# Kernel optimization log

Measured on AMD Instinct MI355X. Metric: run time of the kernel, lower is better.

Reference implementation:

```python
import jax, jax.numpy as jnp
import numpy as np


def _nearest(img, cy, cx):
    # PyTorch F.grid_sample(mode='nearest', align_corners=False, padding_mode='zeros').
    # img: [B,C,H,W]; cy,cx: [B,N] normalized coords in [-1,1] (cy->H axis, cx->W axis).
    B, C, H, W = img.shape
    iy = jnp.rint((cy + 1.0) * H / 2.0 - 0.5)  # unnormalize then nearbyint
    ix = jnp.rint((cx + 1.0) * W / 2.0 - 0.5)
    valid = (iy >= 0) & (iy < H) & (ix >= 0) & (ix < W)
    flat = (jnp.clip(iy, 0, H - 1).astype(jnp.int32) * W
            + jnp.clip(ix, 0, W - 1).astype(jnp.int32))  # [B,N]
    g = jnp.take_along_axis(img.reshape(B, C, H * W), flat[:, None, :], axis=2)  # [B,C,N]
    g = jnp.where(valid[:, None, :], g, 0.0)
    return g.transpose(0, 2, 1)  # [B,N,C]


def setup_inputs() -> dict:
    key = jax.random.key(0)
    ks = jax.random.split(key, 16)
    B, N = 2, 16384
    h, w = 64, 64       # LR feat / lr_guide resolution
    H, W = 256, 256     # HR guide resolution
    Cf, Cg = 128, 128   # feat_dim, guide_dim
    inp = {
        'feat': jax.random.normal(ks[0], (B, Cf, h, w), jnp.float32),
        'coord': jax.random.uniform(ks[1], (B, N, 2), jnp.float32) * 2.0 - 1.0,
        'hr_guide': jax.random.normal(ks[2], (B, Cg, H, W), jnp.float32),
        'lr_guide': jax.random.normal(ks[3], (B, Cg, h, w), jnp.float32),
    }
    dims = [386, 1024, 512, 256, 128, 2]  # imnet_in_dim -> hidden_list -> out_dim
    for i in range(5):
        fan_in, fan_out = dims[i], dims[i + 1]
        scale = np.sqrt(2.0 / fan_in).astype(np.float32)
        inp[f'W{i}'] = jax.random.normal(ks[4 + i], (fan_out, fan_in), jnp.float32) * scale
        inp[f'b{i}'] = jnp.zeros((fan_out,), jnp.float32)
    return inp


def reference(feat, coord, hr_guide, lr_guide, W0, b0, W1, b1, W2, b2, W3, b3, W4, b4):
    b, c, h, w = feat.shape
    # make_coord((h,w), flatten=False).permute(2,0,1): channel 0 = y (h axis), 1 = x (w axis)
    ys = -1.0 + 2.0 * (jnp.arange(h, dtype=jnp.float32) + 0.5) / h
    xs = -1.0 + 2.0 * (jnp.arange(w, dtype=jnp.float32) + 0.5) / w
    fc = jnp.stack([jnp.broadcast_to(ys[:, None], (h, w)),
                    jnp.broadcast_to(xs[None, :], (h, w))], 0)[None]  # [1,2,h,w]
    fc = jnp.broadcast_to(fc, (b, 2, h, w))

    # coord.flip(-1) as grid -> grid x = coord[...,1] (W axis), grid y = coord[...,0] (H axis)
    q_guide_hr = _nearest(hr_guide, coord[..., 0], coord[..., 1])  # [B,N,Cg]

    # 4 offsets (vx,vy) in [-1,1]x[-1,1], scaled by rx=1/h, ry=1/w (loop order of torch code)
    offs = jnp.array([[-1., -1.], [-1., 1.], [1., -1.], [1., 1.]], jnp.float32)
    offs = offs * jnp.array([1.0 / h, 1.0 / w], jnp.float32)
    cK = coord[None] + offs[:, None, None, :]  # [4,B,N,2]

    samp = jax.vmap(_nearest, in_axes=(None, 0, 0))
    q_feat = samp(feat, cK[..., 0], cK[..., 1])      # [4,B,N,Cf]
    q_coord = samp(fc, cK[..., 0], cK[..., 1])       # [4,B,N,2]
    q_lr = samp(lr_guide, cK[..., 0], cK[..., 1])    # [4,B,N,Cg]

    rel = (coord[None] - q_coord) * jnp.array([float(h), float(w)], jnp.float32)  # [4,B,N,2]
    qg_hr = jnp.broadcast_to(q_guide_hr[None], q_lr.shape)
    inp = jnp.concatenate([q_feat, qg_hr, qg_hr - q_lr, rel], axis=-1)  # [4,B,N,386]

    x = inp
    for Wl, bl in ((W0, b0), (W1, b1), (W2, b2), (W3, b3)):
        x = jax.nn.relu(x @ Wl.T + bl)
    preds = x @ W4.T + b4                      # [4,B,N,2]
    preds = jnp.moveaxis(preds, 0, -1)         # [B,N,2,4]
    wgt = jax.nn.softmax(preds[:, :, 1, :], axis=-1)
    return jnp.sum(preds[:, :, 0, :] * wgt, axis=-1, keepdims=True)  # [B,N,1]
```

## Files before the change

kernel.cpp:

```cpp
#include <hip/hip_runtime.h>
#include <cstdint>

typedef __attribute__((ext_vector_type(8))) _Float16 half8;
typedef __attribute__((ext_vector_type(16))) float   f32x16;

#define BN 2
#define NN 16384
#define FH 64
#define FW 64
#define GH 256
#define GW 256
#define CC 128
#define M_TOTAL (4*BN*NN)
#define MROWS 64
#define NBLK (M_TOTAL/MROWS)

#define SX  456
#define SHC 520
#define S2H 520
#define S3  264
#define S4  136
#define OFF_HC 29184
#define OFF_H3 62464
#define LDS_ELEMS 79360

#define MFMA(a,b,c) __builtin_amdgcn_mfma_f32_32x32x16_f16((a),(b),(c),0,0,0)

static __device__ __forceinline__ f32x16 zero16() {
  f32x16 z;
#pragma unroll
  for (int i = 0; i < 16; ++i) z[i] = 0.f;
  return z;
}
static __device__ __forceinline__ half8 zero8() {
  half8 z;
#pragma unroll
  for (int e = 0; e < 8; ++e) z[e] = (_Float16)0.f;
  return z;
}

template<int NB>
static __device__ __forceinline__ void ldA2(half8 (&A0)[NB], half8 (&A1)[NB],
    const _Float16* wa, const _Float16* wb, int t) {
#pragma unroll
  for (int i = 0; i < NB; ++i) {
    const int kt = t * NB + i;
    A0[i] = *(const half8*)(wa + kt * 512);
    A1[i] = *(const half8*)(wb + kt * 512);
  }
}
template<int NB>
static __device__ __forceinline__ void ldA1(half8 (&A)[NB], const _Float16* wa, int t) {
#pragma unroll
  for (int i = 0; i < NB; ++i) A[i] = *(const half8*)(wa + (t * NB + i) * 512);
}
template<int NB>
static __device__ __forceinline__ void ldB2(half8 (&B0)[NB], half8 (&B1)[NB],
    const _Float16* p0, const _Float16* p1, int t) {
#pragma unroll
  for (int i = 0; i < NB; ++i) {
    const int kt = t * NB + i;
    B0[i] = *(const half8*)(p0 + kt * 16);
    B1[i] = *(const half8*)(p1 + kt * 16);
  }
}
template<int NB>
static __device__ __forceinline__ void ldB1(half8 (&B)[NB], const _Float16* p, int t) {
#pragma unroll
  for (int i = 0; i < NB; ++i) B[i] = *(const half8*)(p + (t * NB + i) * 16);
}

template<int NB>
static __device__ __forceinline__ void mm_22(f32x16& a00, f32x16& a01, f32x16& a10, f32x16& a11,
    const half8 (&A0)[NB], const half8 (&A1)[NB], const half8 (&B0)[NB], const half8 (&B1)[NB]) {
  __builtin_amdgcn_sched_barrier(0);
  __builtin_amdgcn_s_setprio(1);
#pragma unroll
  for (int i = 0; i < NB; ++i) {
    a00 = MFMA(A0[i], B0[i], a00);
    a01 = MFMA(A0[i], B1[i], a01);
    a10 = MFMA(A1[i], B0[i], a10);
    a11 = MFMA(A1[i], B1[i], a11);
  }
  __builtin_amdgcn_s_setprio(0);
  __builtin_amdgcn_sched_barrier(0);
}
template<int NB>
static __device__ __forceinline__ void mm_12(f32x16& lo, f32x16& hi,
    const half8 (&A)[NB], const half8 (&B0)[NB], const half8 (&B1)[NB]) {
  __builtin_amdgcn_sched_barrier(0);
  __builtin_amdgcn_s_setprio(1);
#pragma unroll
  for (int i = 0; i < NB; ++i) {
    lo = MFMA(A[i], B0[i], lo);
    hi = MFMA(A[i], B1[i], hi);
  }
  __builtin_amdgcn_s_setprio(0);
  __builtin_amdgcn_sched_barrier(0);
}
template<int NB>
static __device__ __forceinline__ void mm_11(f32x16& acc,
    const half8 (&A)[NB], const half8 (&B)[NB]) {
  __builtin_amdgcn_sched_barrier(0);
  __builtin_amdgcn_s_setprio(1);
#pragma unroll
  for (int i = 0; i < NB; ++i) acc = MFMA(A[i], B[i], acc);
  __builtin_amdgcn_s_setprio(0);
  __builtin_amdgcn_sched_barrier(0);
}

__global__ void pack_w(const float* __restrict__ wsrc, _Float16* __restrict__ out,
                       int NT, int K, int KT) {
  int idx = blockIdx.x * 256 + threadIdx.x;
  int total = NT * KT * 64;
  if (idx >= total) return;
  int l = idx & 63;
  int t = idx >> 6;
  int kt = t % KT;
  int jt = t / KT;
  int row = jt * 32 + (l & 31);
  int k0 = kt * 16 + (l >> 5) * 8;
  _Float16* o = out + (size_t)idx * 8;
#pragma unroll
  for (int e = 0; e < 8; ++e) {
    int k = k0 + e;
    float v = (k < K) ? wsrc[(size_t)row * K + k] : 0.f;
    o[e] = (_Float16)v;
  }
}

__global__ void transpose_to_hwc(const float* __restrict__ in, _Float16* __restrict__ out,
                                 int C, int HH, int WW) {
  __shared__ float tile[32][33];
  const int xt = blockIdx.x, ct = blockIdx.y;
  const int bb = blockIdx.z / HH, y = blockIdx.z % HH;
  const int tx = threadIdx.x, ty = threadIdx.y;
  const int x0 = xt * 32, c0 = ct * 32;
#pragma unroll
  for (int i = 0; i < 4; ++i) {
    int c = c0 + ty + i * 8;
    tile[ty + i * 8][tx] = in[((size_t)(bb * C + c) * HH + y) * WW + x0 + tx];
  }
  __syncthreads();
#pragma unroll
  for (int i = 0; i < 4; ++i) {
    int x = x0 + ty + i * 8;
    out[((size_t)(bb * HH + y) * WW + x) * C + c0 + tx] = (_Float16)tile[tx][ty + i * 8];
  }
}

template<bool RELU>
static __device__ __forceinline__ void store_tile(const f32x16 acc, _Float16* lout, int ldo,
                                                  int row0, int col0,
                                                  const float* __restrict__ biasBase, int lane) {
  const int m = row0 + (lane & 31);
  const int s4 = (lane >> 5) * 4;
  _Float16* rp = lout + (size_t)m * ldo + col0 + s4;
  const float* bp = biasBase + s4;
#pragma unroll
  for (int g = 0; g < 4; ++g) {
    float4 bv = *(const float4*)(bp + 8 * g);
    union { _Float16 h[4]; unsigned long long u; } pk;
#pragma unroll
    for (int e = 0; e < 4; ++e) {
      float v = acc[4 * g + e] + ((const float*)&bv)[e];
      if (RELU) v = fmaxf(v, 0.f);
      pk.h[e] = (_Float16)v;
    }
    *(unsigned long long*)(rp + 8 * g) = pk.u;
  }
}

__global__ __launch_bounds__(512, 2) void jiif_main(
    const float* __restrict__ coord,
    const _Float16* __restrict__ featT, const _Float16* __restrict__ hrT,
    const _Float16* __restrict__ lrT,
    const _Float16* __restrict__ W0p, const _Float16* __restrict__ W1p,
    const _Float16* __restrict__ W2p, const _Float16* __restrict__ W3p,
    const float* __restrict__ b0, const float* __restrict__ b1,
    const float* __restrict__ b2, const float* __restrict__ b3,
    const float* __restrict__ W4, const float* __restrict__ b4,
    float* __restrict__ preds) {
  extern __shared__ _Float16 lds[];
  const int tid = threadIdx.x;
  const int w = tid >> 6, lane = tid & 63;
  const int m0 = blockIdx.x * MROWS;
  _Float16* X   = lds;
  _Float16* Hc  = lds + OFF_HC;
  _Float16* H2r = lds;
  _Float16* H3r = lds + OFF_H3;
  _Float16* H4r = lds;

  {
    const int r = tid >> 3;
    const int g = tid & 7;
    const int row = m0 + r;
    const int n = row & (NN - 1);
    const int bb = (row >> 14) & (BN - 1);
    const int k = row >> 15;
    const float c0 = coord[((size_t)bb * NN + n) * 2 + 0];
    const float c1 = coord[((size_t)bb * NN + n) * 2 + 1];
    const float cy = c0 + ((k < 2) ? -1.f : 1.f) * (1.f / FH);
    const float cx = c1 + ((k & 1) ? 1.f : -1.f) * (1.f / FW);
    const float fy = rintf((cy + 1.f) * (FH * 0.5f) - 0.5f);
    const float fx = rintf((cx + 1.f) * (FW * 0.5f) - 0.5f);
    const bool vF = (fy >= 0.f) && (fy < (float)FH) && (fx >= 0.f) && (fx < (float)FW);
    const int iy = max(0, min(FH - 1, (int)fy));
    const int ix = max(0, min(FW - 1, (int)fx));
    const float gy = rintf((c0 + 1.f) * (GH * 0.5f) - 0.5f);
    const float gx = rintf((c1 + 1.f) * (GW * 0.5f) - 0.5f);
    const bool vH = (gy >= 0.f) && (gy < (float)GH) && (gx >= 0.f) && (gx < (float)GW);
    const int jy = max(0, min(GH - 1, (int)gy));
    const int jx = max(0, min(GW - 1, (int)gx));
    const _Float16* fp = featT + (size_t)((bb * FH + iy) * FW + ix) * CC;
    const _Float16* lp = lrT  + (size_t)((bb * FH + iy) * FW + ix) * CC;
    const _Float16* hp = hrT  + (size_t)((bb * GH + jy) * GW + jx) * CC;
    _Float16* xr = X + (size_t)r * SX;
#pragma unroll
    for (int t = 0; t < 2; ++t) {
      const int c8 = g * 16 + t * 8;
      half8 fv = vF ? *(const half8*)(fp + c8) : zero8();
      half8 lv = vF ? *(const half8*)(lp + c8) : zero8();
      half8 hv = vH ? *(const half8*)(hp + c8) : zero8();
      *(half8*)(xr + c8) = fv;
      *(half8*)(xr + CC + c8) = hv;
      half8 dv = hv - lv;
      *(half8*)(xr + 2 * CC + c8) = dv;
    }
    *(unsigned long long*)(xr + 384 + g * 8) = 0ull;
    *(unsigned long long*)(xr + 384 + g * 8 + 4) = 0ull;
    if (g == 0) {
      const float qc0 = vF ? (-1.f + (float)(2 * iy + 1) * (1.f / FH)) : 0.f;
      const float qc1 = vF ? (-1.f + (float)(2 * ix + 1) * (1.f / FW)) : 0.f;
      xr[384] = (_Float16)((c0 - qc0) * (float)FH);
      xr[385] = (_Float16)((c1 - qc1) * (float)FW);
    }
  }
  __syncthreads();

  const int m31 = lane & 31;
  const int s8 = (lane >> 5) * 8;
  const _Float16* xb0 = X + (size_t)m31 * SX + s8;
  const _Float16* xb1 = xb0 + 32 * SX;
  const _Float16* hb0 = Hc + (size_t)m31 * SHC + s8;
  const _Float16* hb1 = hb0 + 32 * SHC;

  {
    f32x16 a00 = zero16(), a01 = zero16(), a10 = zero16(), a11 = zero16();
    const _Float16* wa = W0p + ((size_t)(2 * w) * 28 * 64 + lane) * 8;
    const _Float16* wb = wa + 28 * 512;
    half8 pA0[2], pA1[2], pB0[2], pB1[2], qA0[2], qA1[2], qB0[2], qB1[2];
    ldA2<2>(pA0, pA1, wa, wb, 0); ldB2<2>(pB0, pB1, xb0, xb1, 0);
    ldA2<2>(qA0, qA1, wa, wb, 1); ldB2<2>(qB0, qB1, xb0, xb1, 1);
#pragma unroll 1
    for (int u = 0; u < 6; ++u) {
      mm_22<2>(a00, a01, a10, a11, pA0, pA1, pB0, pB1);
      ldA2<2>(pA0, pA1, wa, wb, 2 * u + 2); ldB2<2>(pB0, pB1, xb0, xb1, 2 * u + 2);
      mm_22<2>(a00, a01, a10, a11, qA0, qA1, qB0, qB1);
      ldA2<2>(qA0, qA1, wa, wb, 2 * u + 3); ldB2<2>(qB0, qB1, xb0, xb1, 2 * u + 3);
    }
    mm_22<2>(a00, a01, a10, a11, pA0, pA1, pB0, pB1);
    mm_22<2>(a00, a01, a10, a11, qA0, qA1, qB0, qB1);
    store_tile<true>(a00, Hc, SHC, 0,  (2 * w) * 32,     b0 + (2 * w) * 32,     lane);
    store_tile<true>(a01, Hc, SHC, 32, (2 * w) * 32,     b0 + (2 * w) * 32,     lane);
    store_tile<true>(a10, Hc, SHC, 0,  (2 * w + 1) * 32, b0 + (2 * w + 1) * 32, lane);
    store_tile<true>(a11, Hc, SHC, 32, (2 * w + 1) * 32, b0 + (2 * w + 1) * 32, lane);
  }
  __syncthreads();

  f32x16 a2_00 = zero16(), a2_01 = zero16(), a2_10 = zero16(), a2_11 = zero16();
  const _Float16* w1a = W1p + ((size_t)(2 * w) * 64 * 64 + lane) * 8;
  const _Float16* w1b = w1a + 64 * 512;
  {
    half8 sA0[2], sA1[2], sB0[2], sB1[2], tA0[2], tA1[2], tB0[2], tB1[2];
    ldA2<2>(sA0, sA1, w1a, w1b, 0); ldB2<2>(sB0, sB1, hb0, hb1, 0);
    ldA2<2>(tA0, tA1, w1a, w1b, 1); ldB2<2>(tB0, tB1, hb0, hb1, 1);
#pragma unroll 1
    for (int u = 0; u < 7; ++u) {
      mm_22<2>(a2_00, a2_01, a2_10, a2_11, sA0, sA1, sB0, sB1);
      ldA2<2>(sA0, sA1, w1a, w1b, 2 * u + 2); ldB2<2>(sB0, sB1, hb0, hb1, 2 * u + 2);
      mm_22<2>(a2_00, a2_01, a2_10, a2_11, tA0, tA1, tB0, tB1);
      ldA2<2>(tA0, tA1, w1a, w1b, 2 * u + 3); ldB2<2>(tB0, tB1, hb0, hb1, 2 * u + 3);
    }
    mm_22<2>(a2_00, a2_01, a2_10, a2_11, sA0, sA1, sB0, sB1);
    mm_22<2>(a2_00, a2_01, a2_10, a2_11, tA0, tA1, tB0, tB1);
  }
  __syncthreads();

  {
    f32x16 a00 = zero16(), a01 = zero16(), a10 = zero16(), a11 = zero16();
    const _Float16* wa = W0p + ((size_t)(16 + 2 * w) * 28 * 64 + lane) * 8;
    const _Float16* wb = wa + 28 * 512;
    half8 pA0[2], pA1[2], pB0[2], pB1[2], qA0[2], qA1[2], qB0[2], qB1[2];
    ldA2<2>(pA0, pA1, wa, wb, 0); ldB2<2>(pB0, pB1, xb0, xb1, 0);
    ldA2<2>(qA0, qA1, wa, wb, 1); ldB2<2>(qB0, qB1, xb0, xb1, 1);
#pragma unroll 1
    for (int u = 0; u < 6; ++u) {
      mm_22<2>(a00, a01, a10, a11, pA0, pA1, pB0, pB1);
      ldA2<2>(pA0, pA1, wa, wb, 2 * u + 2); ldB2<2>(pB0, pB1, xb0, xb1, 2 * u + 2);
      mm_22<2>(a00, a01, a10, a11, qA0, qA1, qB0, qB1);
      ldA2<2>(qA0, qA1, wa, wb, 2 * u + 3); ldB2<2>(qB0, qB1, xb0, xb1, 2 * u + 3);
    }
    mm_22<2>(a00, a01, a10, a11, pA0, pA1, pB0, pB1);
    mm_22<2>(a00, a01, a10, a11, qA0, qA1, qB0, qB1);
    store_tile<true>(a00, Hc, SHC, 0,  (2 * w) * 32,     b0 + 512 + (2 * w) * 32,     lane);
    store_tile<true>(a01, Hc, SHC, 32, (2 * w) * 32,     b0 + 512 + (2 * w) * 32,     lane);
    store_tile<true>(a10, Hc, SHC, 0,  (2 * w + 1) * 32, b0 + 512 + (2 * w + 1) * 32, lane);
    store_tile<true>(a11, Hc, SHC, 32, (2 * w + 1) * 32, b0 + 512 + (2 * w + 1) * 32, lane);
  }
  __syncthreads();

  {
    const _Float16* wa = w1a + 32 * 512;
    const _Float16* wb = w1b + 32 * 512;
    half8 sA0[2], sA1[2], sB0[2], sB1[2], tA0[2], tA1[2], tB0[2], tB1[2];
    ldA2<2>(sA0, sA1, wa, wb, 0); ldB2<2>(sB0, sB1, hb0, hb1, 0);
    ldA2<2>(tA0, tA1, wa, wb, 1); ldB2<2>(tB0, tB1, hb0, hb1, 1);
#pragma unroll 1
    for (int u = 0; u < 7; ++u) {
      mm_22<2>(a2_00, a2_01, a2_10, a2_11, sA0, sA1, sB0, sB1);
      ldA2<2>(sA0, sA1, wa, wb, 2 * u + 2); ldB2<2>(sB0, sB1, hb0, hb1, 2 * u + 2);
      mm_22<2>(a2_00, a2_01, a2_10, a2_11, tA0, tA1, tB0, tB1);
      ldA2<2>(tA0, tA1, wa, wb, 2 * u + 3); ldB2<2>(tB0, tB1, hb0, hb1, 2 * u + 3);
    }
    mm_22<2>(a2_00, a2_01, a2_10, a2_11, sA0, sA1, sB0, sB1);
    mm_22<2>(a2_00, a2_01, a2_10, a2_11, tA0, tA1, tB0, tB1);
  }
  __syncthreads();

  store_tile<true>(a2_00, H2r, S2H, 0,  (2 * w) * 32,     b1 + (2 * w) * 32,     lane);
  store_tile<true>(a2_01, H2r, S2H, 32, (2 * w) * 32,     b1 + (2 * w) * 32,     lane);
  store_tile<true>(a2_10, H2r, S2H, 0,  (2 * w + 1) * 32, b1 + (2 * w + 1) * 32, lane);
  store_tile<true>(a2_11, H2r, S2H, 32, (2 * w + 1) * 32, b1 + (2 * w + 1) * 32, lane);
  __syncthreads();

  {
    const _Float16* wb2 = W2p + ((size_t)w * 32 * 64 + lane) * 8;
    const _Float16* h2b0 = H2r + (size_t)m31 * S2H + s8;
    const _Float16* h2b1 = h2b0 + 32 * S2H;
    f32x16 a3lo = zero16(), a3hi = zero16();
    half8 sA[2], sB0[2], sB1[2], tA[2], tB0[2], tB1[2];
    ldA1<2>(sA, wb2, 0); ldB2<2>(sB0, sB1, h2b0, h2b1, 0);
    ldA1<2>(tA, wb2, 1); ldB2<2>(tB0, tB1, h2b0, h2b1, 1);
#pragma unroll 1
    for (int u = 0; u < 7; ++u) {
      mm_12<2>(a3lo, a3hi, sA, sB0, sB1);
      ldA1<2>(sA, wb2, 2 * u + 2); ldB2<2>(sB0, sB1, h2b0, h2b1, 2 * u + 2);
      mm_12<2>(a3lo, a3hi, tA, tB0, tB1);
      ldA1<2>(tA, wb2, 2 * u + 3); ldB2<2>(tB0, tB1, h2b0, h2b1, 2 * u + 3);
    }
    mm_12<2>(a3lo, a3hi, sA, sB0, sB1);
    mm_12<2>(a3lo, a3hi, tA, tB0, tB1);
    store_tile<true>(a3lo, H3r, S3, 0,  w * 32, b2 + w * 32, lane);
    store_tile<true>(a3hi, H3r, S3, 32, w * 32, b2 + w * 32, lane);
  }
  __syncthreads();

  {
    const int j3 = w & 3, mts = w >> 2;
    const _Float16* wb3 = W3p + ((size_t)j3 * 16 * 64 + lane) * 8;
    const _Float16* h3b = H3r + (size_t)(mts * 32 + m31) * S3 + s8;
    f32x16 a4 = zero16();
    half8 sA[4], sB[4], tA[4], tB[4];
    ldA1<4>(sA, wb3, 0); ldB1<4>(sB, h3b, 0);
    ldA1<4>(tA, wb3, 1); ldB1<4>(tB, h3b, 1);
    mm_11<4>(a4, sA, sB);
    ldA1<4>(sA, wb3, 2); ldB1<4>(sB, h3b, 2);
    mm_11<4>(a4, tA, tB);
    ldA1<4>(tA, wb3, 3); ldB1<4>(tB, h3b, 3);
    mm_11<4>(a4, sA, sB);
    mm_11<4>(a4, tA, tB);
    store_tile<true>(a4, H4r, S4, mts * 32, j3 * 32, b3 + j3 * 32, lane);
  }
  __syncthreads();

  {
    const int m = tid >> 3;
    const int sub = tid & 7;
    const int j = sub & 1;
    const int q = sub >> 1;
    const _Float16* h4 = H4r + (size_t)m * S4 + q * 32;
    const float* w4 = W4 + j * CC + q * 32;
    float s = 0.f;
#pragma unroll
    for (int cc = 0; cc < 32; ++cc) s += (float)h4[cc] * w4[cc];
    s += __shfl_xor(s, 2);
    s += __shfl_xor(s, 4);
    if (q == 0) preds[(size_t)(m0 + m) * 2 + j] = s + b4[j];
  }
}

__global__ void jiif_combine(const float* __restrict__ preds, float* __restrict__ out) {
  const int i = blockIdx.x * 256 + threadIdx.x;
  if (i >= BN * NN) return;
  float p0[4], p1[4];
#pragma unroll
  for (int k = 0; k < 4; ++k) {
    p0[k] = preds[((size_t)k * BN * NN + i) * 2 + 0];
    p1[k] = preds[((size_t)k * BN * NN + i) * 2 + 1];
  }
  float mx = fmaxf(fmaxf(p1[0], p1[1]), fmaxf(p1[2], p1[3]));
  float se = 0.f, so = 0.f;
#pragma unroll
  for (int k = 0; k < 4; ++k) {
    float e = expf(p1[k] - mx);
    se += e;
    so += p0[k] * e;
  }
  out[i] = so / se;
}

extern "C" void kernel_launch(void* const* d_in, const int* in_sizes, int n_in,
                              void* d_out, int out_size, void* d_ws, size_t ws_size,
                              hipStream_t stream) {
  const float* feat  = (const float*)d_in[0];
  const float* coord = (const float*)d_in[1];
  const float* hr    = (const float*)d_in[2];
  const float* lr    = (const float*)d_in[3];
  const float* W0 = (const float*)d_in[4];  const float* b0 = (const float*)d_in[5];
  const float* W1 = (const float*)d_in[6];  const float* b1 = (const float*)d_in[7];
  const float* W2 = (const float*)d_in[8];  const float* b2 = (const float*)d_in[9];
  const float* W3 = (const float*)d_in[10]; const float* b3 = (const float*)d_in[11];
  const float* W4 = (const float*)d_in[12]; const float* b4 = (const float*)d_in[13];

  char* ws = (char*)d_ws;
  _Float16* W0p   = (_Float16*)(ws + 0);
  _Float16* W1p   = (_Float16*)(ws + 917504);
  _Float16* W2p   = (_Float16*)(ws + 1966080);
  _Float16* W3p   = (_Float16*)(ws + 2228224);
  _Float16* featT = (_Float16*)(ws + 2293760);
  _Float16* hrT   = (_Float16*)(ws + 4390912);
  _Float16* lrT   = (_Float16*)(ws + 37945344);
  float* preds    = (float*)(ws + 40042496);
  if (ws_size < 41091072) return;

  pack_w<<<224, 256, 0, stream>>>(W0, W0p, 32, 386, 28);
  pack_w<<<256, 256, 0, stream>>>(W1, W1p, 16, 1024, 64);
  pack_w<<<64,  256, 0, stream>>>(W2, W2p, 8, 512, 32);
  pack_w<<<16,  256, 0, stream>>>(W3, W3p, 4, 256, 16);

  transpose_to_hwc<<<dim3(2, 4, 128), dim3(32, 8), 0, stream>>>(feat, featT, CC, FH, FW);
  transpose_to_hwc<<<dim3(8, 4, 512), dim3(32, 8), 0, stream>>>(hr,   hrT,   CC, GH, GW);
  transpose_to_hwc<<<dim3(2, 4, 128), dim3(32, 8), 0, stream>>>(lr,   lrT,   CC, FH, FW);

  (void)hipFuncSetAttribute((const void*)jiif_main,
                            hipFuncAttributeMaxDynamicSharedMemorySize, LDS_ELEMS * 2);
  jiif_main<<<NBLK, 512, LDS_ELEMS * 2, stream>>>(
      coord, featT, hrT, lrT, W0p, W1p, W2p, W3p, b0, b1, b2, b3, W4, b4, preds);

  jiif_combine<<<(BN * NN + 255) / 256, 256, 0, stream>>>(preds, (float*)d_out);
}
```

Measured before the change: 357.1 us.

## Double block to 1024 threads, give each wave one output column tile

The fused MLP block grows from 8 to 16 waves. Each wave now computes a single 32-column tile per layer instead of two, with mm_12 replacing mm_22. Layer 2 is split across both M halves, and the gather and final dot product are remapped to 16 threads per row. The aim is more waves to hide latency per block. The cost is that each weight fragment is reused across fewer MFMAs, so global weight loads per FLOP double, and occupancy moves from 2 blocks per CU to 1.

Result: slower. 434.4 us (+21.6%).

```diff
diff --git a/kernel.cpp b/kernel.cpp
--- a/kernel.cpp
+++ b/kernel.cpp
@@ -40,16 +40,6 @@
 }
 
 template<int NB>
-static __device__ __forceinline__ void ldA2(half8 (&A0)[NB], half8 (&A1)[NB],
-    const _Float16* wa, const _Float16* wb, int t) {
-#pragma unroll
-  for (int i = 0; i < NB; ++i) {
-    const int kt = t * NB + i;
-    A0[i] = *(const half8*)(wa + kt * 512);
-    A1[i] = *(const half8*)(wb + kt * 512);
-  }
-}
-template<int NB>
 static __device__ __forceinline__ void ldA1(half8 (&A)[NB], const _Float16* wa, int t) {
 #pragma unroll
   for (int i = 0; i < NB; ++i) A[i] = *(const half8*)(wa + (t * NB + i) * 512);
@@ -70,21 +60,6 @@
   for (int i = 0; i < NB; ++i) B[i] = *(const half8*)(p + (t * NB + i) * 16);
 }
 
-template<int NB>
-static __device__ __forceinline__ void mm_22(f32x16& a00, f32x16& a01, f32x16& a10, f32x16& a11,
-    const half8 (&A0)[NB], const half8 (&A1)[NB], const half8 (&B0)[NB], const half8 (&B1)[NB]) {
-  __builtin_amdgcn_sched_barrier(0);
-  __builtin_amdgcn_s_setprio(1);
-#pragma unroll
-  for (int i = 0; i < NB; ++i) {
-    a00 = MFMA(A0[i], B0[i], a00);
-    a01 = MFMA(A0[i], B1[i], a01);
-    a10 = MFMA(A1[i], B0[i], a10);
-    a11 = MFMA(A1[i], B1[i], a11);
-  }
-  __builtin_amdgcn_s_setprio(0);
-  __builtin_amdgcn_sched_barrier(0);
-}
 template<int NB>
 static __device__ __forceinline__ void mm_12(f32x16& lo, f32x16& hi,
     const half8 (&A)[NB], const half8 (&B0)[NB], const half8 (&B1)[NB]) {
@@ -171,7 +146,7 @@
   }
 }
 
-__global__ __launch_bounds__(512, 2) void jiif_main(
+__global__ __launch_bounds__(1024, 1) void jiif_main(
     const float* __restrict__ coord,
     const _Float16* __restrict__ featT, const _Float16* __restrict__ hrT,
     const _Float16* __restrict__ lrT,
@@ -192,8 +167,8 @@
   _Float16* H4r = lds;
 
   {
-    const int r = tid >> 3;
-    const int g = tid & 7;
+    const int r = tid >> 4;
+    const int g = tid & 15;
     const int row = m0 + r;
     const int n = row & (NN - 1);
     const int bb = (row >> 14) & (BN - 1);
@@ -216,19 +191,18 @@
     const _Float16* lp = lrT  + (size_t)((bb * FH + iy) * FW + ix) * CC;
     const _Float16* hp = hrT  + (size_t)((bb * GH + jy) * GW + jx) * CC;
     _Float16* xr = X + (size_t)r * SX;
-#pragma unroll
-    for (int t = 0; t < 2; ++t) {
-      const int c8 = g * 16 + t * 8;
-      half8 fv = vF ? *(const half8*)(fp + c8) : zero8();
-      half8 lv = vF ? *(const half8*)(lp + c8) : zero8();
-      half8 hv = vH ? *(const half8*)(hp + c8) : zero8();
-      *(half8*)(xr + c8) = fv;
-      *(half8*)(xr + CC + c8) = hv;
-      half8 dv = hv - lv;
-      *(half8*)(xr + 2 * CC + c8) = dv;
-    }
-    *(unsigned long long*)(xr + 384 + g * 8) = 0ull;
-    *(unsigned long long*)(xr + 384 + g * 8 + 4) = 0ull;
+    const int c8 = g * 8;
+    half8 fv = vF ? *(const half8*)(fp + c8) : zero8();
+    half8 lv = vF ? *(const half8*)(lp + c8) : zero8();
+    half8 hv = vH ? *(const half8*)(hp + c8) : zero8();
+    *(half8*)(xr + c8) = fv;
+    *(half8*)(xr + CC + c8) = hv;
+    half8 dv = hv - lv;
+    *(half8*)(xr + 2 * CC + c8) = dv;
+    if (g < 8) {
+      *(unsigned long long*)(xr + 384 + g * 8) = 0ull;
+      *(unsigned long long*)(xr + 384 + g * 8 + 4) = 0ull;
+    }
     if (g == 0) {
       const float qc0 = vF ? (-1.f + (float)(2 * iy + 1) * (1.f / FH)) : 0.f;
       const float qc1 = vF ? (-1.f + (float)(2 * ix + 1) * (1.f / FW)) : 0.f;
@@ -245,121 +219,111 @@
   const _Float16* hb0 = Hc + (size_t)m31 * SHC + s8;
   const _Float16* hb1 = hb0 + 32 * SHC;
 
-  {
-    f32x16 a00 = zero16(), a01 = zero16(), a10 = zero16(), a11 = zero16();
-    const _Float16* wa = W0p + ((size_t)(2 * w) * 28 * 64 + lane) * 8;
-    const _Float16* wb = wa + 28 * 512;
-    half8 pA0[2], pA1[2], pB0[2], pB1[2], qA0[2], qA1[2], qB0[2], qB1[2];
-    ldA2<2>(pA0, pA1, wa, wb, 0); ldB2<2>(pB0, pB1, xb0, xb1, 0);
-    ldA2<2>(qA0, qA1, wa, wb, 1); ldB2<2>(qB0, qB1, xb0, xb1, 1);
+  f32x16 a2_0 = zero16(), a2_1 = zero16();
+  const _Float16* w1a = W1p + ((size_t)w * 64 * 64 + lane) * 8;
+
+  {
+    f32x16 a0 = zero16(), a1 = zero16();
+    const _Float16* wa = W0p + ((size_t)w * 28 * 64 + lane) * 8;
+    half8 sA[2], sB0[2], sB1[2], tA[2], tB0[2], tB1[2];
+    ldA1<2>(sA, wa, 0); ldB2<2>(sB0, sB1, xb0, xb1, 0);
+    ldA1<2>(tA, wa, 1); ldB2<2>(tB0, tB1, xb0, xb1, 1);
 #pragma unroll 1
     for (int u = 0; u < 6; ++u) {
-      mm_22<2>(a00, a01, a10, a11, pA0, pA1, pB0, pB1);
-      ldA2<2>(pA0, pA1, wa, wb, 2 * u + 2); ldB2<2>(pB0, pB1, xb0, xb1, 2 * u + 2);
-      mm_22<2>(a00, a01, a10, a11, qA0, qA1, qB0, qB1);
-      ldA2<2>(qA0, qA1, wa, wb, 2 * u + 3); ldB2<2>(qB0, qB1, xb0, xb1, 2 * u + 3);
-    }
-    mm_22<2>(a00, a01, a10, a11, pA0, pA1, pB0, pB1);
-    mm_22<2>(a00, a01, a10, a11, qA0, qA1, qB0, qB1);
-    store_tile<true>(a00, Hc, SHC, 0,  (2 * w) * 32,     b0 + (2 * w) * 32,     lane);
-    store_tile<true>(a01, Hc, SHC, 32, (2 * w) * 32,     b0 + (2 * w) * 32,     lane);
-    store_tile<true>(a10, Hc, SHC, 0,  (2 * w + 1) * 32, b0 + (2 * w + 1) * 32, lane);
-    store_tile<true>(a11, Hc, SHC, 32, (2 * w + 1) * 32, b0 + (2 * w + 1) * 32, lane);
-  }
-  __syncthreads();
-
-  f32x16 a2_00 = zero16(), a2_01 = zero16(), a2_10 = zero16(), a2_11 = zero16();
-  const _Float16* w1a = W1p + ((size_t)(2 * w) * 64 * 64 + lane) * 8;
-  const _Float16* w1b = w1a + 64 * 512;
-  {
-    half8 sA0[2], sA1[2], sB0[2], sB1[2], tA0[2], tA1[2], tB0[2], tB1[2];
-    ldA2<2>(sA0, sA1, w1a, w1b, 0); ldB2<2>(sB0, sB1, hb0, hb1, 0);
-    ldA2<2>(tA0, tA1, w1a, w1b, 1); ldB2<2>(tB0, tB1, hb0, hb1, 1);
+      mm_12<2>(a0, a1, sA, sB0, sB1);
+      ldA1<2>(sA, wa, 2 * u + 2); ldB2<2>(sB0, sB1, xb0, xb1, 2 * u + 2);
+      mm_12<2>(a0, a1, tA, tB0, tB1);
+      ldA1<2>(tA, wa, 2 * u + 3); ldB2<2>(tB0, tB1, xb0, xb1, 2 * u + 3);
+    }
+    mm_12<2>(a0, a1, sA, sB0, sB1);
+    mm_12<2>(a0, a1, tA, tB0, tB1);
+    store_tile<true>(a0, Hc, SHC, 0,  w * 32, b0 + w * 32, lane);
+    store_tile<true>(a1, Hc, SHC, 32, w * 32, b0 + w * 32, lane);
+  }
+  __syncthreads();
+
+  {
+    half8 sA[2], sB0[2], sB1[2], tA[2], tB0[2], tB1[2];
+    ldA1<2>(sA, w1a, 0); ldB2<2>(sB0, sB1, hb0, hb1, 0);
+    ldA1<2>(tA, w1a, 1); ldB2<2>(tB0, tB1, hb0, hb1, 1);
 #pragma unroll 1
     for (int u = 0; u < 7; ++u) {
-      mm_22<2>(a2_00, a2_01, a2_10, a2_11, sA0, sA1, sB0, sB1);
-      ldA2<2>(sA0, sA1, w1a, w1b, 2 * u + 2); ldB2<2>(sB0, sB1, hb0, hb1, 2 * u + 2);
-      mm_22<2>(a2_00, a2_01, a2_10, a2_11, tA0, tA1, tB0, tB1);
-      ldA2<2>(tA0, tA1, w1a, w1b, 2 * u + 3); ldB2<2>(tB0, tB1, hb0, hb1, 2 * u + 3);
-    }
-    mm_22<2>(a2_00, a2_01, a2_10, a2_11, sA0, sA1, sB0, sB1);
-    mm_22<2>(a2_00, a2_01, a2_10, a2_11, tA0, tA1, tB0, tB1);
-  }
-  __syncthreads();
-
-  {
-    f32x16 a00 = zero16(), a01 = zero16(), a10 = zero16(), a11 = zero16();
-    const _Float16* wa = W0p + ((size_t)(16 + 2 * w) * 28 * 64 + lane) * 8;
-    const _Float16* wb = wa + 28 * 512;
-    half8 pA0[2], pA1[2], pB0[2], pB1[2], qA0[2], qA1[2], qB0[2], qB1[2];
-    ldA2<2>(pA0, pA1, wa, wb, 0); ldB2<2>(pB0, pB1, xb0, xb1, 0);
-    ldA2<2>(qA0, qA1, wa, wb, 1); ldB2<2>(qB0, qB1, xb0, xb1, 1);
+      mm_12<2>(a2_0, a2_1, sA, sB0, sB1);
+      ldA1<2>(sA, w1a, 2 * u + 2); ldB2<2>(sB0, sB1, hb0, hb1, 2 * u + 2);
+      mm_12<2>(a2_0, a2_1, tA, tB0, tB1);
+      ldA1<2>(tA, w1a, 2 * u + 3); ldB2<2>(tB0, tB1, hb0, hb1, 2 * u + 3);
+    }
+    mm_12<2>(a2_0, a2_1, sA, sB0, sB1);
+    mm_12<2>(a2_0, a2_1, tA, tB0, tB1);
+  }
+  __syncthreads();
+
+  {
+    f32x16 a0 = zero16(), a1 = zero16();
+    const _Float16* wa = W0p + ((size_t)(16 + w) * 28 * 64 + lane) * 8;
+    half8 sA[2], sB0[2], sB1[2], tA[2], tB0[2], tB1[2];
+    ldA1<2>(sA, wa, 0); ldB2<2>(sB0, sB1, xb0, xb1, 0);
+    ldA1<2>(tA, wa, 1); ldB2<2>(tB0, tB1, xb0, xb1, 1);
 #pragma unroll 1
     for (int u = 0; u < 6; ++u) {
-      mm_22<2>(a00, a01, a10, a11, pA0, pA1, pB0, pB1);
-      ldA2<2>(pA0, pA1, wa, wb, 2 * u + 2); ldB2<2>(pB0, pB1, xb0, xb1, 2 * u + 2);
-      mm_22<2>(a00, a01, a10, a11, qA0, qA1, qB0, qB1);
-      ldA2<2>(qA0, qA1, wa, wb, 2 * u + 3); ldB2<2>(qB0, qB1, xb0, xb1, 2 * u + 3);
-    }
-    mm_22<2>(a00, a01, a10, a11, pA0, pA1, pB0, pB1);
-    mm_22<2>(a00, a01, a10, a11, qA0, qA1, qB0, qB1);
-    store_tile<true>(a00, Hc, SHC, 0,  (2 * w) * 32,     b0 + 512 + (2 * w) * 32,     lane);
-    store_tile<true>(a01, Hc, SHC, 32, (2 * w) * 32,     b0 + 512 + (2 * w) * 32,     lane);
-    store_tile<true>(a10, Hc, SHC, 0,  (2 * w + 1) * 32, b0 + 512 + (2 * w + 1) * 32, lane);
-    store_tile<true>(a11, Hc, SHC, 32, (2 * w + 1) * 32, b0 + 512 + (2 * w + 1) * 32, lane);
+      mm_12<2>(a0, a1, sA, sB0, sB1);
+      ldA1<2>(sA, wa, 2 * u + 2); ldB2<2>(sB0, sB1, xb0, xb1, 2 * u + 2);
+      mm_12<2>(a0, a1, tA, tB0, tB1);
+      ldA1<2>(tA, wa, 2 * u + 3); ldB2<2>(tB0, tB1, xb0, xb1, 2 * u + 3);
+    }
+    mm_12<2>(a0, a1, sA, sB0, sB1);
+    mm_12<2>(a0, a1, tA, tB0, tB1);
+    store_tile<true>(a0, Hc, SHC, 0,  w * 32, b0 + 512 + w * 32, lane);
+    store_tile<true>(a1, Hc, SHC, 32, w * 32, b0 + 512 + w * 32, lane);
   }
   __syncthreads();
 
   {
     const _Float16* wa = w1a + 32 * 512;
-    const _Float16* wb = w1b + 32 * 512;
-    half8 sA0[2], sA1[2], sB0[2], sB1[2], tA0[2], tA1[2], tB0[2], tB1[2];
-    ldA2<2>(sA0, sA1, wa, wb, 0); ldB2<2>(sB0, sB1, hb0, hb1, 0);
-    ldA2<2>(tA0, tA1, wa, wb, 1); ldB2<2>(tB0, tB1, hb0, hb1, 1);
+    half8 sA[2], sB0[2], sB1[2], tA[2], tB0[2], tB1[2];
+    ldA1<2>(sA, wa, 0); ldB2<2>(sB0, sB1, hb0, hb1, 0);
+    ldA1<2>(tA, wa, 1); ldB2<2>(tB0, tB1, hb0, hb1, 1);
 #pragma unroll 1
     for (int u = 0; u < 7; ++u) {
-      mm_22<2>(a2_00, a2_01, a2_10, a2_11, sA0, sA1, sB0, sB1);
-      ldA2<2>(sA0, sA1, wa, wb, 2 * u + 2); ldB2<2>(sB0, sB1, hb0, hb1, 2 * u + 2);
-      mm_22<2>(a2_00, a2_01, a2_10, a2_11, tA0, tA1, tB0, tB1);
-      ldA2<2>(tA0, tA1, wa, wb, 2 * u + 3); ldB2<2>(tB0, tB1, hb0, hb1, 2 * u + 3);
-    }
-    mm_22<2>(a2_00, a2_01, a2_10, a2_11, sA0, sA1, sB0, sB1);
-    mm_22<2>(a2_00, a2_01, a2_10, a2_11, tA0, tA1, tB0, tB1);
-  }
-  __syncthreads();
-
-  store_tile<true>(a2_00, H2r, S2H, 0,  (2 * w) * 32,     b1 + (2 * w) * 32,     lane);
-  store_tile<true>(a2_01, H2r, S2H, 32, (2 * w) * 32,     b1 + (2 * w) * 32,     lane);
-  store_tile<true>(a2_10, H2r, S2H, 0,  (2 * w + 1) * 32, b1 + (2 * w + 1) * 32, lane);
-  store_tile<true>(a2_11, H2r, S2H, 32, (2 * w + 1) * 32, b1 + (2 * w + 1) * 32, lane);
-  __syncthreads();
-
-  {
-    const _Float16* wb2 = W2p + ((size_t)w * 32 * 64 + lane) * 8;
-    const _Float16* h2b0 = H2r + (size_t)m31 * S2H + s8;
-    const _Float16* h2b1 = h2b0 + 32 * S2H;
-    f32x16 a3lo = zero16(), a3hi = zero16();
-    half8 sA[2], sB0[2], sB1[2], tA[2], tB0[2], tB1[2];
-    ldA1<2>(sA, wb2, 0); ldB2<2>(sB0, sB1, h2b0, h2b1, 0);
-    ldA1<2>(tA, wb2, 1); ldB2<2>(tB0, tB1, h2b0, h2b1, 1);
+      mm_12<2>(a2_0, a2_1, sA, sB0, sB1);
+      ldA1<2>(sA, wa, 2 * u + 2); ldB2<2>(sB0, sB1, hb0, hb1, 2 * u + 2);
+      mm_12<2>(a2_0, a2_1, tA, tB0, tB1);
+      ldA1<2>(tA, wa, 2 * u + 3); ldB2<2>(tB0, tB1, hb0, hb1, 2 * u + 3);
+    }
+    mm_12<2>(a2_0, a2_1, sA, sB0, sB1);
+    mm_12<2>(a2_0, a2_1, tA, tB0, tB1);
+  }
+  __syncthreads();
+
+  store_tile<true>(a2_0, H2r, S2H, 0,  w * 32, b1 + w * 32, lane);
+  store_tile<true>(a2_1, H2r, S2H, 32, w * 32, b1 + w * 32, lane);
+  __syncthreads();
+
+  {
+    const _Float16* wb2 = W2p + ((size_t)(w & 7) * 32 * 64 + lane) * 8;
+    const int mts2 = w >> 3;
+    const _Float16* h2b = H2r + (size_t)(mts2 * 32 + m31) * S2H + s8;
+    f32x16 a3 = zero16();
+    half8 sA[2], sB[2], tA[2], tB[2];
+    ldA1<2>(sA, wb2, 0); ldB1<2>(sB, h2b, 0);
+    ldA1<2>(tA, wb2, 1); ldB1<2>(tB, h2b, 1);
 #pragma unroll 1
     for (int u = 0; u < 7; ++u) {
-      mm_12<2>(a3lo, a3hi, sA, sB0, sB1);
-      ldA1<2>(sA, wb2, 2 * u + 2); ldB2<2>(sB0, sB1, h2b0, h2b1, 2 * u + 2);
-      mm_12<2>(a3lo, a3hi, tA, tB0, tB1);
-      ldA1<2>(tA, wb2, 2 * u + 3); ldB2<2>(tB0, tB1, h2b0, h2b1, 2 * u + 3);
-    }
-    mm_12<2>(a3lo, a3hi, sA, sB0, sB1);
-    mm_12<2>(a3lo, a3hi, tA, tB0, tB1);
-    store_tile<true>(a3lo, H3r, S3, 0,  w * 32, b2 + w * 32, lane);
-    store_tile<true>(a3hi, H3r, S3, 32, w * 32, b2 + w * 32, lane);
-  }
-  __syncthreads();
-
-  {
-    const int j3 = w & 3, mts = w >> 2;
+      mm_11<2>(a3, sA, sB);
+      ldA1<2>(sA, wb2, 2 * u + 2); ldB1<2>(sB, h2b, 2 * u + 2);
+      mm_11<2>(a3, tA, tB);
+      ldA1<2>(tA, wb2, 2 * u + 3); ldB1<2>(tB, h2b, 2 * u + 3);
+    }
+    mm_11<2>(a3, sA, sB);
+    mm_11<2>(a3, tA, tB);
+    store_tile<true>(a3, H3r, S3, mts2 * 32, (w & 7) * 32, b2 + (w & 7) * 32, lane);
+  }
+  __syncthreads();
+
+  if (w < 8) {
+    const int j3 = w & 3, mts3 = w >> 2;
     const _Float16* wb3 = W3p + ((size_t)j3 * 16 * 64 + lane) * 8;
-    const _Float16* h3b = H3r + (size_t)(mts * 32 + m31) * S3 + s8;
+    const _Float16* h3b = H3r + (size_t)(mts3 * 32 + m31) * S3 + s8;
     f32x16 a4 = zero16();
     half8 sA[4], sB[4], tA[4], tB[4];
     ldA1<4>(sA, wb3, 0); ldB1<4>(sB, h3b, 0);
@@ -370,22 +334,23 @@
     ldA1<4>(tA, wb3, 3); ldB1<4>(tB, h3b, 3);
     mm_11<4>(a4, sA, sB);
     mm_11<4>(a4, tA, tB);
-    store_tile<true>(a4, H4r, S4, mts * 32, j3 * 32, b3 + j3 * 32, lane);
-  }
-  __syncthreads();
-
-  {
-    const int m = tid >> 3;
-    const int sub = tid & 7;
+    store_tile<true>(a4, H4r, S4, mts3 * 32, j3 * 32, b3 + j3 * 32, lane);
+  }
+  __syncthreads();
+
+  {
+    const int m = tid >> 4;
+    const int sub = tid & 15;
     const int j = sub & 1;
     const int q = sub >> 1;
-    const _Float16* h4 = H4r + (size_t)m * S4 + q * 32;
-    const float* w4 = W4 + j * CC + q * 32;
+    const _Float16* h4 = H4r + (size_t)m * S4 + q * 16;
+    const float* w4 = W4 + j * CC + q * 16;
     float s = 0.f;
 #pragma unroll
-    for (int cc = 0; cc < 32; ++cc) s += (float)h4[cc] * w4[cc];
+    for (int cc = 0; cc < 16; ++cc) s += (float)h4[cc] * w4[cc];
     s += __shfl_xor(s, 2);
     s += __shfl_xor(s, 4);
+    s += __shfl_xor(s, 8);
     if (q == 0) preds[(size_t)(m0 + m) * 2 + j] = s + b4[j];
   }
 }
@@ -445,7 +410,7 @@
 
   (void)hipFuncSetAttribute((const void*)jiif_main,
                             hipFuncAttributeMaxDynamicSharedMemorySize, LDS_ELEMS * 2);
-  jiif_main<<<NBLK, 512, LDS_ELEMS * 2, stream>>>(
+  jiif_main<<<NBLK, 1024, LDS_ELEMS * 2, stream>>>(
       coord, featT, hrT, lrT, W0p, W1p, W2p, W3p, b0, b1, b2, b3, W4, b4, preds);
 
   jiif_combine<<<(BN * NN + 255) / 256, 256, 0, stream>>>(preds, (float*)d_out);
```

## Stage layer-0/1 weight tiles via global_load_lds double buffer instead of registers

Applied to the files above, without the earlier changes.

Weight A-fragments for the first two MLP layers now stream from global memory directly into a per-wave LDS staging double buffer using global_load_lds, then get read from LDS, rather than being loaded into registers two k-steps ahead. The two chunk passes are folded into one loop over c, and waits use explicit vmcnt counters. The aim is to cut VGPR pressure and overlap weight fetch with MFMA work. The cost is extra LDS traffic, an extra LDS read per step, and a shallower prefetch of one k-step at a time, which may expose global latency.

After: 388.5 us. 1.09x slower.

```diff
diff --git a/kernel.cpp b/kernel.cpp
--- a/kernel.cpp
+++ b/kernel.cpp
@@ -39,16 +39,13 @@
   return z;
 }
 
-template<int NB>
-static __device__ __forceinline__ void ldA2(half8 (&A0)[NB], half8 (&A1)[NB],
-    const _Float16* wa, const _Float16* wb, int t) {
-#pragma unroll
-  for (int i = 0; i < NB; ++i) {
-    const int kt = t * NB + i;
-    A0[i] = *(const half8*)(wa + kt * 512);
-    A1[i] = *(const half8*)(wb + kt * 512);
-  }
-}
+typedef __attribute__((address_space(1))) const void gas_void;
+typedef __attribute__((address_space(3))) void las_void;
+static __device__ __forceinline__ void glds16(const _Float16* g, const _Float16* l) {
+  __builtin_amdgcn_global_load_lds((gas_void*)(uintptr_t)g,
+                                   (las_void*)(uint32_t)(uintptr_t)l, 16, 0, 0);
+}
+
 template<int NB>
 static __device__ __forceinline__ void ldA1(half8 (&A)[NB], const _Float16* wa, int t) {
 #pragma unroll
@@ -70,21 +67,6 @@
   for (int i = 0; i < NB; ++i) B[i] = *(const half8*)(p + (t * NB + i) * 16);
 }
 
-template<int NB>
-static __device__ __forceinline__ void mm_22(f32x16& a00, f32x16& a01, f32x16& a10, f32x16& a11,
-    const half8 (&A0)[NB], const half8 (&A1)[NB], const half8 (&B0)[NB], const half8 (&B1)[NB]) {
-  __builtin_amdgcn_sched_barrier(0);
-  __builtin_amdgcn_s_setprio(1);
-#pragma unroll
-  for (int i = 0; i < NB; ++i) {
-    a00 = MFMA(A0[i], B0[i], a00);
-    a01 = MFMA(A0[i], B1[i], a01);
-    a10 = MFMA(A1[i], B0[i], a10);
-    a11 = MFMA(A1[i], B1[i], a11);
-  }
-  __builtin_amdgcn_s_setprio(0);
-  __builtin_amdgcn_sched_barrier(0);
-}
 template<int NB>
 static __device__ __forceinline__ void mm_12(f32x16& lo, f32x16& hi,
     const half8 (&A)[NB], const half8 (&B0)[NB], const half8 (&B1)[NB]) {
@@ -190,6 +172,7 @@
   _Float16* H2r = lds;
   _Float16* H3r = lds + OFF_H3;
   _Float16* H4r = lds;
+  _Float16* stg = lds + OFF_H3 + (size_t)w * 2048;
 
   {
     const int r = tid >> 3;
@@ -240,93 +223,123 @@
 
   const int m31 = lane & 31;
   const int s8 = (lane >> 5) * 8;
+  const int lane8 = lane * 8;
   const _Float16* xb0 = X + (size_t)m31 * SX + s8;
   const _Float16* xb1 = xb0 + 32 * SX;
   const _Float16* hb0 = Hc + (size_t)m31 * SHC + s8;
   const _Float16* hb1 = hb0 + 32 * SHC;
 
-  {
-    f32x16 a00 = zero16(), a01 = zero16(), a10 = zero16(), a11 = zero16();
-    const _Float16* wa = W0p + ((size_t)(2 * w) * 28 * 64 + lane) * 8;
-    const _Float16* wb = wa + 28 * 512;
-    half8 pA0[2], pA1[2], pB0[2], pB1[2], qA0[2], qA1[2], qB0[2], qB1[2];
-    ldA2<2>(pA0, pA1, wa, wb, 0); ldB2<2>(pB0, pB1, xb0, xb1, 0);
-    ldA2<2>(qA0, qA1, wa, wb, 1); ldB2<2>(qB0, qB1, xb0, xb1, 1);
-#pragma unroll 1
-    for (int u = 0; u < 6; ++u) {
-      mm_22<2>(a00, a01, a10, a11, pA0, pA1, pB0, pB1);
-      ldA2<2>(pA0, pA1, wa, wb, 2 * u + 2); ldB2<2>(pB0, pB1, xb0, xb1, 2 * u + 2);
-      mm_22<2>(a00, a01, a10, a11, qA0, qA1, qB0, qB1);
-      ldA2<2>(qA0, qA1, wa, wb, 2 * u + 3); ldB2<2>(qB0, qB1, xb0, xb1, 2 * u + 3);
-    }
-    mm_22<2>(a00, a01, a10, a11, pA0, pA1, pB0, pB1);
-    mm_22<2>(a00, a01, a10, a11, qA0, qA1, qB0, qB1);
-    store_tile<true>(a00, Hc, SHC, 0,  (2 * w) * 32,     b0 + (2 * w) * 32,     lane);
-    store_tile<true>(a01, Hc, SHC, 32, (2 * w) * 32,     b0 + (2 * w) * 32,     lane);
-    store_tile<true>(a10, Hc, SHC, 0,  (2 * w + 1) * 32, b0 + (2 * w + 1) * 32, lane);
-    store_tile<true>(a11, Hc, SHC, 32, (2 * w + 1) * 32, b0 + (2 * w + 1) * 32, lane);
-  }
-  __syncthreads();
-
   f32x16 a2_00 = zero16(), a2_01 = zero16(), a2_10 = zero16(), a2_11 = zero16();
   const _Float16* w1a = W1p + ((size_t)(2 * w) * 64 * 64 + lane) * 8;
   const _Float16* w1b = w1a + 64 * 512;
-  {
-    half8 sA0[2], sA1[2], sB0[2], sB1[2], tA0[2], tA1[2], tB0[2], tB1[2];
-    ldA2<2>(sA0, sA1, w1a, w1b, 0); ldB2<2>(sB0, sB1, hb0, hb1, 0);
-    ldA2<2>(tA0, tA1, w1a, w1b, 1); ldB2<2>(tB0, tB1, hb0, hb1, 1);
+
 #pragma unroll 1
-    for (int u = 0; u < 7; ++u) {
-      mm_22<2>(a2_00, a2_01, a2_10, a2_11, sA0, sA1, sB0, sB1);
-      ldA2<2>(sA0, sA1, w1a, w1b, 2 * u + 2); ldB2<2>(sB0, sB1, hb0, hb1, 2 * u + 2);
-      mm_22<2>(a2_00, a2_01, a2_10, a2_11, tA0, tA1, tB0, tB1);
-      ldA2<2>(tA0, tA1, w1a, w1b, 2 * u + 3); ldB2<2>(tB0, tB1, hb0, hb1, 2 * u + 3);
-    }
-    mm_22<2>(a2_00, a2_01, a2_10, a2_11, sA0, sA1, sB0, sB1);
-    mm_22<2>(a2_00, a2_01, a2_10, a2_11, tA0, tA1, tB0, tB1);
-  }
-  __syncthreads();
-
-  {
+  for (int c = 0; c < 2; ++c) {
     f32x16 a00 = zero16(), a01 = zero16(), a10 = zero16(), a11 = zero16();
-    const _Float16* wa = W0p + ((size_t)(16 + 2 * w) * 28 * 64 + lane) * 8;
+    const _Float16* wa = W0p + ((size_t)(c * 16 + 2 * w) * 28 * 64 + lane) * 8;
     const _Float16* wb = wa + 28 * 512;
-    half8 pA0[2], pA1[2], pB0[2], pB1[2], qA0[2], qA1[2], qB0[2], qB1[2];
-    ldA2<2>(pA0, pA1, wa, wb, 0); ldB2<2>(pB0, pB1, xb0, xb1, 0);
-    ldA2<2>(qA0, qA1, wa, wb, 1); ldB2<2>(qB0, qB1, xb0, xb1, 1);
+    glds16(wa, stg);            glds16(wb, stg + 512);
+    glds16(wa + 512, stg + 1024); glds16(wb + 512, stg + 1536);
+    half8 B0c = *(const half8*)(xb0);
+    half8 B1c = *(const half8*)(xb1);
 #pragma unroll 1
-    for (int u = 0; u < 6; ++u) {
-      mm_22<2>(a00, a01, a10, a11, pA0, pA1, pB0, pB1);
-      ldA2<2>(pA0, pA1, wa, wb, 2 * u + 2); ldB2<2>(pB0, pB1, xb0, xb1, 2 * u + 2);
-      mm_22<2>(a00, a01, a10, a11, qA0, qA1, qB0, qB1);
-      ldA2<2>(qA0, qA1, wa, wb, 2 * u + 3); ldB2<2>(qB0, qB1, xb0, xb1, 2 * u + 3);
-    }
-    mm_22<2>(a00, a01, a10, a11, pA0, pA1, pB0, pB1);
-    mm_22<2>(a00, a01, a10, a11, qA0, qA1, qB0, qB1);
-    store_tile<true>(a00, Hc, SHC, 0,  (2 * w) * 32,     b0 + 512 + (2 * w) * 32,     lane);
-    store_tile<true>(a01, Hc, SHC, 32, (2 * w) * 32,     b0 + 512 + (2 * w) * 32,     lane);
-    store_tile<true>(a10, Hc, SHC, 0,  (2 * w + 1) * 32, b0 + 512 + (2 * w + 1) * 32, lane);
-    store_tile<true>(a11, Hc, SHC, 32, (2 * w + 1) * 32, b0 + 512 + (2 * w + 1) * 32, lane);
-  }
-  __syncthreads();
-
-  {
-    const _Float16* wa = w1a + 32 * 512;
-    const _Float16* wb = w1b + 32 * 512;
-    half8 sA0[2], sA1[2], sB0[2], sB1[2], tA0[2], tA1[2], tB0[2], tB1[2];
-    ldA2<2>(sA0, sA1, wa, wb, 0); ldB2<2>(sB0, sB1, hb0, hb1, 0);
-    ldA2<2>(tA0, tA1, wa, wb, 1); ldB2<2>(tB0, tB1, hb0, hb1, 1);
+    for (int kt = 0; kt < 26; ++kt) {
+      const int sl = (kt & 1) << 10;
+      asm volatile("s_waitcnt vmcnt(2)" ::: "memory");
+      __builtin_amdgcn_sched_barrier(0);
+      half8 A0 = *(const half8*)(stg + sl + lane8);
+      half8 A1 = *(const half8*)(stg + sl + 512 + lane8);
+      half8 B0n = *(const half8*)(xb0 + (kt + 1) * 16);
+      half8 B1n = *(const half8*)(xb1 + (kt + 1) * 16);
+      __builtin_amdgcn_sched_barrier(0);
+      __builtin_amdgcn_s_setprio(1);
+      a00 = MFMA(A0, B0c, a00); a01 = MFMA(A0, B1c, a01);
+      a10 = MFMA(A1, B0c, a10); a11 = MFMA(A1, B1c, a11);
+      __builtin_amdgcn_s_setprio(0);
+      __builtin_amdgcn_sched_barrier(0);
+      glds16(wa + (kt + 2) * 512, stg + sl);
+      glds16(wb + (kt + 2) * 512, stg + sl + 512);
+      B0c = B0n; B1c = B1n;
+    }
+    {
+      asm volatile("s_waitcnt vmcnt(2)" ::: "memory");
+      __builtin_amdgcn_sched_barrier(0);
+      half8 A0 = *(const half8*)(stg + lane8);
+      half8 A1 = *(const half8*)(stg + 512 + lane8);
+      half8 B0n = *(const half8*)(xb0 + 27 * 16);
+      half8 B1n = *(const half8*)(xb1 + 27 * 16);
+      __builtin_amdgcn_s_setprio(1);
+      a00 = MFMA(A0, B0c, a00); a01 = MFMA(A0, B1c, a01);
+      a10 = MFMA(A1, B0c, a10); a11 = MFMA(A1, B1c, a11);
+      __builtin_amdgcn_s_setprio(0);
+      B0c = B0n; B1c = B1n;
+    }
+    {
+      asm volatile("s_waitcnt vmcnt(0)" ::: "memory");
+      __builtin_amdgcn_sched_barrier(0);
+      half8 A0 = *(const half8*)(stg + 1024 + lane8);
+      half8 A1 = *(const half8*)(stg + 1536 + lane8);
+      __builtin_amdgcn_s_setprio(1);
+      a00 = MFMA(A0, B0c, a00); a01 = MFMA(A0, B1c, a01);
+      a10 = MFMA(A1, B0c, a10); a11 = MFMA(A1, B1c, a11);
+      __builtin_amdgcn_s_setprio(0);
+    }
+    store_tile<true>(a00, Hc, SHC, 0,  (2 * w) * 32,     b0 + c * 512 + (2 * w) * 32,     lane);
+    store_tile<true>(a01, Hc, SHC, 32, (2 * w) * 32,     b0 + c * 512 + (2 * w) * 32,     lane);
+    store_tile<true>(a10, Hc, SHC, 0,  (2 * w + 1) * 32, b0 + c * 512 + (2 * w + 1) * 32, lane);
+    store_tile<true>(a11, Hc, SHC, 32, (2 * w + 1) * 32, b0 + c * 512 + (2 * w + 1) * 32, lane);
+    __syncthreads();
+
+    const _Float16* wla = w1a + c * 32 * 512;
+    const _Float16* wlb = w1b + c * 32 * 512;
+    glds16(wla, stg);             glds16(wlb, stg + 512);
+    glds16(wla + 512, stg + 1024); glds16(wlb + 512, stg + 1536);
+    B0c = *(const half8*)(hb0);
+    B1c = *(const half8*)(hb1);
 #pragma unroll 1
-    for (int u = 0; u < 7; ++u) {
-      mm_22<2>(a2_00, a2_01, a2_10, a2_11, sA0, sA1, sB0, sB1);
-      ldA2<2>(sA0, sA1, wa, wb, 2 * u + 2); ldB2<2>(sB0, sB1, hb0, hb1, 2 * u + 2);
-      mm_22<2>(a2_00, a2_01, a2_10, a2_11, tA0, tA1, tB0, tB1);
-      ldA2<2>(tA0, tA1, wa, wb, 2 * u + 3); ldB2<2>(tB0, tB1, hb0, hb1, 2 * u + 3);
-    }
-    mm_22<2>(a2_00, a2_01, a2_10, a2_11, sA0, sA1, sB0, sB1);
-    mm_22<2>(a2_00, a2_01, a2_10, a2_11, tA0, tA1, tB0, tB1);
-  }
-  __syncthreads();
+    for (int kt = 0; kt < 30; ++kt) {
+      const int sl = (kt & 1) << 10;
+      asm volatile("s_waitcnt vmcnt(2)" ::: "memory");
+      __builtin_amdgcn_sched_barrier(0);
+      half8 A0 = *(const half8*)(stg + sl + lane8);
+      half8 A1 = *(const half8*)(stg + sl + 512 + lane8);
+      half8 B0n = *(const half8*)(hb0 + (kt + 1) * 16);
+      half8 B1n = *(const half8*)(hb1 + (kt + 1) * 16);
+      __builtin_amdgcn_sched_barrier(0);
+      __builtin_amdgcn_s_setprio(1);
+      a2_00 = MFMA(A0, B0c, a2_00); a2_01 = MFMA(A0, B1c, a2_01);
+      a2_10 = MFMA(A1, B0c, a2_10); a2_11 = MFMA(A1, B1c, a2_11);
+      __builtin_amdgcn_s_setprio(0);
+      __builtin_amdgcn_sched_barrier(0);
+      glds16(wla + (kt + 2) * 512, stg + sl);
+      glds16(wlb + (kt + 2) * 512, stg + sl + 512);
+      B0c = B0n; B1c = B1n;
+    }
+    {
+      asm volatile("s_waitcnt vmcnt(2)" ::: "memory");
+      __builtin_amdgcn_sched_barrier(0);
+      half8 A0 = *(const half8*)(stg + lane8);
+      half8 A1 = *(const half8*)(stg + 512 + lane8);
+      half8 B0n = *(const half8*)(hb0 + 31 * 16);
+      half8 B1n = *(const half8*)(hb1 + 31 * 16);
+      __builtin_amdgcn_s_setprio(1);
+      a2_00 = MFMA(A0, B0c, a2_00); a2_01 = MFMA(A0, B1c, a2_01);
+      a2_10 = MFMA(A1, B0c, a2_10); a2_11 = MFMA(A1, B1c, a2_11);
+      __builtin_amdgcn_s_setprio(0);
+      B0c = B0n; B1c = B1n;
+    }
+    {
+      asm volatile("s_waitcnt vmcnt(0)" ::: "memory");
+      __builtin_amdgcn_sched_barrier(0);
+      half8 A0 = *(const half8*)(stg + 1024 + lane8);
+      half8 A1 = *(const half8*)(stg + 1536 + lane8);
+      __builtin_amdgcn_s_setprio(1);
+      a2_00 = MFMA(A0, B0c, a2_00); a2_01 = MFMA(A0, B1c, a2_01);
+      a2_10 = MFMA(A1, B0c, a2_10); a2_11 = MFMA(A1, B1c, a2_11);
+      __builtin_amdgcn_s_setprio(0);
+    }
+    __syncthreads();
+  }
 
   store_tile<true>(a2_00, H2r, S2H, 0,  (2 * w) * 32,     b1 + (2 * w) * 32,     lane);
   store_tile<true>(a2_01, H2r, S2H, 32, (2 * w) * 32,     b1 + (2 * w) * 32,     lane);
```
